# Optimization experiments

Measured on AMD Instinct MI355X. Metric: run time of the kernel, lower is better.

The kernel has to match this reference:

```python
import jax, jax.numpy as jnp
import numpy as np

SCALE = 1.0 / np.sqrt(512.0).astype(np.float32)  # attention() hardcodes d_k=512


def setup_inputs() -> dict:
    key = jax.random.key(0)
    ks = jax.random.split(key, 9)
    B, S, D = 4, 2048, 512
    mk = lambda k, shape: jax.random.normal(k, shape, dtype=jnp.float32) * 0.05
    return {
        "q": mk(ks[0], (B, S, D)),
        "k": mk(ks[1], (B, S, D)),
        "v": mk(ks[2], (B, S, D)),
        "WQ_w": mk(ks[3], (D, D)),
        "WQ_b": mk(ks[4], (D,)),
        "WK_w": mk(ks[5], (D, D)),
        "WK_b": mk(ks[6], (D,)),
        "WV_w": mk(ks[7], (D, D)),
        "WV_b": mk(ks[8], (D,)),
    }


def reference(q, k, v, WQ_w, WQ_b, WK_w, WK_b, WV_w, WV_b):
    # torch nn.Linear: y = x @ W.T + b
    qp = q @ WQ_w.T + WQ_b  # [B,S,dk]
    kp = k @ WK_w.T + WK_b  # [B,S,dk]
    vp = v @ WV_w.T + WV_b  # [B,S,dv]
    qk = jnp.einsum("bqd,bkd->bqk", qp, kp) * SCALE  # [B,Sq,Sk]
    S = qk.shape[1]
    tril = jnp.tril(jnp.ones((S, S), dtype=qk.dtype))  # multiplicative causal mask
    qk = qk * tril
    # NOTE: original applies softmax over dim=1 (the query axis), faithfully kept.
    attn = jax.nn.softmax(qk, axis=1)
    out = jnp.einsum("bqk,bkd->bqd", attn, vp)  # [B,Sq,dv]
    return out
```

## Files before the change

kernel.cpp:

```cpp
#include <hip/hip_runtime.h>
#include <hip/hip_bf16.h>


#define S_LEN 2048
#define D_DIM 512
#define SCALE_F 0.044194173824159216f

typedef __attribute__((ext_vector_type(8))) short s8v;
typedef __attribute__((ext_vector_type(4))) short s4v;
typedef __attribute__((ext_vector_type(4))) float f4v;

enum { EPI_BIAS = 0, EPI_BIAS_T = 1, EPI_SCORES = 2 };

#define SBAR()    asm volatile("s_barrier" ::: "memory")
#define WAITV(n)  asm volatile("s_waitcnt vmcnt(" #n ")" ::: "memory")

__device__ __forceinline__ short f2bf_s(float f) {
  union { __hip_bfloat16 b; short s; } u; u.b = __float2bfloat16(f); return u.s;
}
__device__ __forceinline__ float bf2f_s(short h) {
  union { short s; __hip_bfloat16 b; } u; u.s = h; return __bfloat162float(u.b);
}

__device__ __forceinline__ void glds16(const short* g, short* l) {
  __builtin_amdgcn_global_load_lds((const __attribute__((address_space(1))) void*)g,
                                   (__attribute__((address_space(3))) void*)l, 16, 0, 0);
}

template <int EPI>
__device__ __forceinline__ void gemm_core(
    const short* __restrict__ A, const short* __restrict__ B,
    short* __restrict__ C, const float* __restrict__ bias,
    short* SMEM, int N, int K, size_t sCz, int m0, int n0, int bz,
    float* __restrict__ Z)
{
  const int tid  = threadIdx.x;
  const int w    = tid >> 6;
  const int lane = tid & 63;
  const int quad = lane >> 4;
  const int l16  = lane & 15;
  const int wm   = (w >> 1) * 64;
  const int wn   = (w & 1) * 64;

  const int strow = tid >> 3;
  const int gl = ((tid & 7) ^ (strow & 7)) * 8;

  f4v acc[4][4];
#pragma unroll
  for (int i = 0; i < 4; ++i)
#pragma unroll
    for (int j = 0; j < 4; ++j)
#pragma unroll
      for (int r = 0; r < 4; ++r) acc[i][j][r] = 0.0f;

  const short* Ag = A + (size_t)(m0 + strow) * K + gl;
  const short* Bg = B + (size_t)(n0 + strow) * K + gl;
  const size_t pstr = (size_t)32 * K;
  const int t8 = tid * 8;
  const int swq = l16 & 7;

  const int niter = K >> 6;

#pragma unroll
  for (int p = 0; p < 4; ++p) glds16(Ag + p * pstr, SMEM + t8 + p * 2048);
#pragma unroll
  for (int p = 0; p < 4; ++p) glds16(Bg + p * pstr, SMEM + 8192 + t8 + p * 2048);

  for (int i = 0; i < niter; ++i) {
    const int c = i & 1;
    if (i + 1 < niter) {
      const int k1 = (i + 1) << 6;
      short* dA = SMEM + (1 - c) * 16384 + t8;
#pragma unroll
      for (int p = 0; p < 4; ++p) glds16(Ag + k1 + p * pstr, dA + p * 2048);
#pragma unroll
      for (int p = 0; p < 4; ++p) glds16(Bg + k1 + p * pstr, dA + 8192 + p * 2048);
      WAITV(8);
    } else {
      WAITV(0);
    }
    SBAR();

    const short* As = SMEM + c * 16384;
    const short* Bs = As + 8192;
#pragma unroll
    for (int kk = 0; kk < 2; ++kk) {
      s8v af[4], bf[4];
#pragma unroll
      for (int ii = 0; ii < 4; ++ii)
        af[ii] = *(const s8v*)&As[(wm + ii * 16 + l16) * 64 + (((kk * 4 + quad) ^ swq) * 8)];
#pragma unroll
      for (int j = 0; j < 4; ++j)
        bf[j] = *(const s8v*)&Bs[(wn + j * 16 + l16) * 64 + (((kk * 4 + quad) ^ swq) * 8)];
#pragma unroll
      for (int ii = 0; ii < 4; ++ii)
#pragma unroll
        for (int j = 0; j < 4; ++j)
          acc[ii][j] = __builtin_amdgcn_mfma_f32_16x16x32_bf16(af[ii], bf[j], acc[ii][j], 0, 0, 0);
    }
    SBAR();
  }

  float bv[4];
  if (EPI == EPI_BIAS || EPI == EPI_BIAS_T) {
#pragma unroll
    for (int j = 0; j < 4; ++j) bv[j] = bias[n0 + wn + j * 16 + l16];
  }

  if (EPI == EPI_BIAS_T) {
#pragma unroll
    for (int i = 0; i < 4; ++i) {
#pragma unroll
      for (int j = 0; j < 4; ++j) {
        const int gn  = n0 + wn + j * 16 + l16;
        const int gmb = m0 + wm + i * 16 + quad * 4;
        const int bb = gmb >> 11, ssb = gmb & (S_LEN - 1);
        s4v o;
#pragma unroll
        for (int r = 0; r < 4; ++r) o[r] = f2bf_s(acc[i][j][r] + bv[j]);
        *(s4v*)&C[((size_t)bb * D_DIM + gn) * S_LEN + ssb] = o;
      }
    }
    return;
  }

  short* TB = SMEM;
  const int wbase = w * 2176;
  float csum[4] = {0.f, 0.f, 0.f, 0.f};

#pragma unroll
  for (int ph = 0; ph < 2; ++ph) {
    __syncthreads();
#pragma unroll
    for (int ii = 0; ii < 2; ++ii) {
      const int i = ph * 2 + ii;
#pragma unroll
      for (int j = 0; j < 4; ++j) {
        const int gn = n0 + wn + j * 16 + l16;
#pragma unroll
        for (int r = 0; r < 4; ++r) {
          short o;
          if (EPI == EPI_SCORES) {
            const int gm = m0 + wm + i * 16 + quad * 4 + r;
            const float f = (gm >= gn) ? (__expf(acc[i][j][r] * SCALE_F) - 1.0f) : 0.0f;
            csum[j] += f;
            o = f2bf_s(f);
          } else {
            o = f2bf_s(acc[i][j][r] + bv[j]);
          }
          TB[wbase + (ii * 16 + quad * 4 + r) * 68 + j * 16 + l16] = o;
        }
      }
    }
    __syncthreads();
#pragma unroll
    for (int p = 0; p < 4; ++p) {
      const int row = p * 8 + (lane >> 3);
      const int cg  = lane & 7;
      const s8v vv = *(const s8v*)&TB[wbase + row * 68 + cg * 8];
      const int gm = m0 + wm + ph * 32 + row;
      const int gn = n0 + wn + cg * 8;
      *(s8v*)&C[sCz + (size_t)gm * N + gn] = vv;
    }
  }

  if (EPI == EPI_SCORES) {
#pragma unroll
    for (int j = 0; j < 4; ++j) {
      float cs = csum[j];
      cs += __shfl_xor(cs, 16, 64);
      cs += __shfl_xor(cs, 32, 64);
      if (quad == 0) atomicAdd(&Z[(bz << 11) + n0 + wn + j * 16 + l16], cs);
    }
  }
}

__global__ __launch_bounds__(256, 2) void gemm_scoresF(
    const short* __restrict__ A, const short* __restrict__ B, short* __restrict__ C,
    float* __restrict__ Z)
{
  __shared__ __align__(16) short SMEM[32768];
  const int bz = blockIdx.z;
  const int t = blockIdx.x;
  int ti = (int)((sqrtf(8.0f * t + 1.0f) - 1.0f) * 0.5f);
  while ((ti + 1) * (ti + 2) / 2 <= t) ++ti;
  while (ti * (ti + 1) / 2 > t) --ti;
  const int tj = t - ti * (ti + 1) / 2;
  gemm_core<EPI_SCORES>(A + (size_t)bz * S_LEN * D_DIM, B + (size_t)bz * S_LEN * D_DIM,
                        C, nullptr, SMEM, S_LEN, D_DIM,
                        (size_t)bz * S_LEN * S_LEN, ti * 128, tj * 128, bz, Z);
}

__global__ __launch_bounds__(256, 2) void proj3(
    const short* __restrict__ a0, const short* __restrict__ a1, const short* __restrict__ a2,
    const short* __restrict__ b0, const short* __restrict__ b1, const short* __restrict__ b2,
    short* __restrict__ c0, short* __restrict__ c1, short* __restrict__ c2,
    const float* __restrict__ x0, const float* __restrict__ x1, const float* __restrict__ x2)
{
  __shared__ __align__(16) short SMEM[32768];
  const int z = blockIdx.z;
  const short* A = (z == 0) ? a0 : (z == 1) ? a1 : a2;
  const short* B = (z == 0) ? b0 : (z == 1) ? b1 : b2;
  short*       C = (z == 0) ? c0 : (z == 1) ? c1 : c2;
  const float* bias = (z == 0) ? x0 : (z == 1) ? x1 : x2;
  if (z == 2)
    gemm_core<EPI_BIAS_T>(A, B, C, bias, SMEM, D_DIM, D_DIM, 0,
                          blockIdx.y * 128, blockIdx.x * 128, 0, nullptr);
  else
    gemm_core<EPI_BIAS>(A, B, C, bias, SMEM, D_DIM, D_DIM, 0,
                        blockIdx.y * 128, blockIdx.x * 128, 0, nullptr);
}

__global__ __launch_bounds__(256, 2) void gemm_outF(
    const short* __restrict__ F, const short* __restrict__ vpT,
    const float* __restrict__ Tv, float* __restrict__ out)
{
  __shared__ __align__(16) short SMEM[36864];

  const int tid  = threadIdx.x;
  const int bz   = blockIdx.z;
  const int m0   = (31 - blockIdx.y) * 64;
  const int n0   = blockIdx.x * 128;

  const short* A = F   + (size_t)bz * S_LEN * S_LEN;
  const short* B = vpT + (size_t)bz * D_DIM * S_LEN;

  const int w    = tid >> 6;
  const int lane = tid & 63;
  const int quad = lane >> 4;
  const int l16  = lane & 15;
  const int wm   = (w >> 1) * 32;
  const int wn   = (w & 1) * 64;

  const int strow = tid >> 3;
  const int gl = ((tid & 7) ^ (strow & 7)) * 8;

  f4v acc[2][4];
#pragma unroll
  for (int i = 0; i < 2; ++i)
#pragma unroll
    for (int j = 0; j < 4; ++j)
#pragma unroll
      for (int r = 0; r < 4; ++r) acc[i][j][r] = 0.0f;

  const short* Ag = A + (size_t)(m0 + strow) * S_LEN + gl;
  const short* Bg = B + (size_t)(n0 + strow) * S_LEN + gl;
  const size_t pstr = (size_t)32 * S_LEN;
  const int t8 = tid * 8;
  const int swq = l16 & 7;

  const int niter = (m0 >> 6) + 1;

#pragma unroll
  for (int pre = 0; pre < 2; ++pre) {
    short* dst = SMEM + pre * 12288 + t8;
    const int k0 = pre << 6;
#pragma unroll
    for (int p = 0; p < 2; ++p) glds16(Ag + k0 + p * pstr, dst + p * 2048);
#pragma unroll
    for (int p = 0; p < 4; ++p) glds16(Bg + k0 + p * pstr, dst + 4096 + p * 2048);
  }

  int cbuf = 0, nbuf = 2;
  for (int i = 0; i < niter; ++i) {
    if (i + 2 < niter) {
      const int k2 = (i + 2) << 6;
      short* dst = SMEM + nbuf * 12288 + t8;
#pragma unroll
      for (int p = 0; p < 2; ++p) glds16(Ag + k2 + p * pstr, dst + p * 2048);
#pragma unroll
      for (int p = 0; p < 4; ++p) glds16(Bg + k2 + p * pstr, dst + 4096 + p * 2048);
      nbuf = (nbuf == 2) ? 0 : nbuf + 1;
      WAITV(12);
    } else if (i + 1 < niter) {
      WAITV(6);
    } else {
      WAITV(0);
    }
    SBAR();

    const short* As = SMEM + cbuf * 12288;
    const short* Bs = As + 4096;
    cbuf = (cbuf == 2) ? 0 : cbuf + 1;
#pragma unroll
    for (int kk = 0; kk < 2; ++kk) {
      s8v af[2], bf[4];
#pragma unroll
      for (int ii = 0; ii < 2; ++ii)
        af[ii] = *(const s8v*)&As[(wm + ii * 16 + l16) * 64 + (((kk * 4 + quad) ^ swq) * 8)];
#pragma unroll
      for (int j = 0; j < 4; ++j)
        bf[j] = *(const s8v*)&Bs[(wn + j * 16 + l16) * 64 + (((kk * 4 + quad) ^ swq) * 8)];
#pragma unroll
      for (int ii = 0; ii < 2; ++ii)
#pragma unroll
        for (int j = 0; j < 4; ++j)
          acc[ii][j] = __builtin_amdgcn_mfma_f32_16x16x32_bf16(af[ii], bf[j], acc[ii][j], 0, 0, 0);
    }
    SBAR();
  }

  float* Cf = out + (size_t)bz * S_LEN * D_DIM;
#pragma unroll
  for (int i = 0; i < 2; ++i) {
#pragma unroll
    for (int j = 0; j < 4; ++j) {
      const int gn = n0 + wn + j * 16 + l16;
      const float tvn = Tv[(bz << 9) + gn];
#pragma unroll
      for (int r = 0; r < 4; ++r) {
        const int gm = m0 + wm + i * 16 + quad * 4 + r;
        Cf[(size_t)gm * D_DIM + gn] = acc[i][j][r] + tvn;
      }
    }
  }
}

__global__ __launch_bounds__(256) void cvt3(
    const float* __restrict__ s0, const float* __restrict__ s1,
    const float* __restrict__ s2, short* __restrict__ dst, int n)
{
  const float* s = (blockIdx.y == 0) ? s0 : (blockIdx.y == 1) ? s1 : s2;
  short* d = dst + (size_t)blockIdx.y * n;
  const int i = (blockIdx.x * 256 + threadIdx.x) * 8;
  if (i >= n) return;
  const float4 f0 = *(const float4*)(s + i);
  const float4 f1 = *(const float4*)(s + i + 4);
  s8v o;
  o[0] = f2bf_s(f0.x); o[1] = f2bf_s(f0.y); o[2] = f2bf_s(f0.z); o[3] = f2bf_s(f0.w);
  o[4] = f2bf_s(f1.x); o[5] = f2bf_s(f1.y); o[6] = f2bf_s(f1.z); o[7] = f2bf_s(f1.w);
  *(s8v*)(d + i) = o;
}

__global__ __launch_bounds__(256) void scale_vpt_T(
    short* __restrict__ vpT, const float* __restrict__ ZF, float* __restrict__ Tv)
{
  __shared__ float red[4];
  const int b = blockIdx.y, d = blockIdx.x, tid = threadIdx.x;
  const size_t rowbase = ((size_t)(b * D_DIM + d)) * S_LEN;
  const float* zf = ZF + (b << 11);
  const int k0 = tid * 8;

  s8v v = *(s8v*)&vpT[rowbase + k0];
  float s = 0.0f;
#pragma unroll
  for (int i = 0; i < 8; ++i) {
    const float w = bf2f_s(v[i]) / (2048.0f + zf[k0 + i]);
    s += w;
    v[i] = f2bf_s(w);
  }
  *(s8v*)&vpT[rowbase + k0] = v;

#pragma unroll
  for (int off = 32; off >= 1; off >>= 1) s += __shfl_xor(s, off, 64);
  if ((tid & 63) == 0) red[tid >> 6] = s;
  __syncthreads();
  if (tid == 0) Tv[(b << 9) + d] = red[0] + red[1] + red[2] + red[3];
}

extern "C" void kernel_launch(void* const* d_in, const int* in_sizes, int n_in,
                              void* d_out, int out_size, void* d_ws, size_t ws_size,
                              hipStream_t stream) {
  const float* q   = (const float*)d_in[0];
  const float* k   = (const float*)d_in[1];
  const float* v   = (const float*)d_in[2];
  const float* WQw = (const float*)d_in[3];
  const float* WQb = (const float*)d_in[4];
  const float* WKw = (const float*)d_in[5];
  const float* WKb = (const float*)d_in[6];
  const float* WVw = (const float*)d_in[7];
  const float* WVb = (const float*)d_in[8];

  char* ws = (char*)d_ws;
  short* F   = (short*)(ws);
  short* qb  = (short*)(ws);
  short* Wqb = (short*)(ws + 25165824);
  short* qp  = (short*)(ws + 33554432);
  short* kp  = (short*)(ws + 41943040);
  short* vpT = (short*)(ws + 50331648);
  float* ZF  = (float*)(ws + 58720256);
  float* Tv  = (float*)(ws + 58753024);
  short* kb  = qb + 4194304;
  short* vb  = qb + 8388608;
  short* Wkb = Wqb + 262144;
  short* Wvb = Wqb + 524288;

  const dim3 blk(256);

  hipMemsetAsync(ZF, 0, 4 * S_LEN * sizeof(float), stream);

  cvt3<<<dim3(2048, 3), blk, 0, stream>>>(q, k, v, qb, 4194304);
  cvt3<<<dim3(128, 3), blk, 0, stream>>>(WQw, WKw, WVw, Wqb, 262144);

  proj3<<<dim3(4, 64, 3), blk, 0, stream>>>(
      qb, kb, vb, Wqb, Wkb, Wvb, qp, kp, vpT, WQb, WKb, WVb);

  gemm_scoresF<<<dim3(136, 1, 4), blk, 0, stream>>>(qp, kp, F, ZF);

  scale_vpt_T<<<dim3(512, 4), blk, 0, stream>>>(vpT, ZF, Tv);

  gemm_outF<<<dim3(4, 32, 4), blk, 0, stream>>>(F, vpT, Tv, (float*)d_out);
}
```

Measured before the change: 183.2 us.

## Use 64x128 GEMM tiles, replace atomic column sums with per-tile partials

```diff
diff --git a/kernel.cpp b/kernel.cpp
--- a/kernel.cpp
+++ b/kernel.cpp
@@ -27,27 +27,27 @@
                                    (__attribute__((address_space(3))) void*)l, 16, 0, 0);
 }
 
-template <int EPI>
+template <int EPI, int NI>
 __device__ __forceinline__ void gemm_core(
     const short* __restrict__ A, const short* __restrict__ B,
     short* __restrict__ C, const float* __restrict__ bias,
     short* SMEM, int N, int K, size_t sCz, int m0, int n0, int bz,
-    float* __restrict__ Z)
+    float* __restrict__ ZP)
 {
   const int tid  = threadIdx.x;
   const int w    = tid >> 6;
   const int lane = tid & 63;
   const int quad = lane >> 4;
   const int l16  = lane & 15;
-  const int wm   = (w >> 1) * 64;
+  const int wm   = (w >> 1) * (NI * 16);
   const int wn   = (w & 1) * 64;
 
   const int strow = tid >> 3;
   const int gl = ((tid & 7) ^ (strow & 7)) * 8;
 
-  f4v acc[4][4];
-#pragma unroll
-  for (int i = 0; i < 4; ++i)
+  f4v acc[NI][4];
+#pragma unroll
+  for (int i = 0; i < NI; ++i)
 #pragma unroll
     for (int j = 0; j < 4; ++j)
 #pragma unroll
@@ -58,42 +58,44 @@
   const size_t pstr = (size_t)32 * K;
   const int t8 = tid * 8;
   const int swq = l16 & 7;
+  constexpr int ABUF = NI * 2048;
+  constexpr int BUFS = ABUF + 8192;
 
   const int niter = K >> 6;
 
 #pragma unroll
-  for (int p = 0; p < 4; ++p) glds16(Ag + p * pstr, SMEM + t8 + p * 2048);
-#pragma unroll
-  for (int p = 0; p < 4; ++p) glds16(Bg + p * pstr, SMEM + 8192 + t8 + p * 2048);
+  for (int p = 0; p < NI; ++p) glds16(Ag + p * pstr, SMEM + t8 + p * 2048);
+#pragma unroll
+  for (int p = 0; p < 4; ++p) glds16(Bg + p * pstr, SMEM + ABUF + t8 + p * 2048);
 
   for (int i = 0; i < niter; ++i) {
     const int c = i & 1;
     if (i + 1 < niter) {
       const int k1 = (i + 1) << 6;
-      short* dA = SMEM + (1 - c) * 16384 + t8;
-#pragma unroll
-      for (int p = 0; p < 4; ++p) glds16(Ag + k1 + p * pstr, dA + p * 2048);
-#pragma unroll
-      for (int p = 0; p < 4; ++p) glds16(Bg + k1 + p * pstr, dA + 8192 + p * 2048);
-      WAITV(8);
+      short* dst = SMEM + (1 - c) * BUFS + t8;
+#pragma unroll
+      for (int p = 0; p < NI; ++p) glds16(Ag + k1 + p * pstr, dst + p * 2048);
+#pragma unroll
+      for (int p = 0; p < 4; ++p) glds16(Bg + k1 + p * pstr, dst + ABUF + p * 2048);
+      if constexpr (NI == 4) { WAITV(8); } else { WAITV(6); }
     } else {
       WAITV(0);
     }
     SBAR();
 
-    const short* As = SMEM + c * 16384;
-    const short* Bs = As + 8192;
+    const short* As = SMEM + c * BUFS;
+    const short* Bs = As + ABUF;
 #pragma unroll
     for (int kk = 0; kk < 2; ++kk) {
-      s8v af[4], bf[4];
-#pragma unroll
-      for (int ii = 0; ii < 4; ++ii)
+      s8v af[NI], bf[4];
+#pragma unroll
+      for (int ii = 0; ii < NI; ++ii)
         af[ii] = *(const s8v*)&As[(wm + ii * 16 + l16) * 64 + (((kk * 4 + quad) ^ swq) * 8)];
 #pragma unroll
       for (int j = 0; j < 4; ++j)
         bf[j] = *(const s8v*)&Bs[(wn + j * 16 + l16) * 64 + (((kk * 4 + quad) ^ swq) * 8)];
 #pragma unroll
-      for (int ii = 0; ii < 4; ++ii)
+      for (int ii = 0; ii < NI; ++ii)
 #pragma unroll
         for (int j = 0; j < 4; ++j)
           acc[ii][j] = __builtin_amdgcn_mfma_f32_16x16x32_bf16(af[ii], bf[j], acc[ii][j], 0, 0, 0);
@@ -109,7 +111,7 @@
 
   if (EPI == EPI_BIAS_T) {
 #pragma unroll
-    for (int i = 0; i < 4; ++i) {
+    for (int i = 0; i < NI; ++i) {
 #pragma unroll
       for (int j = 0; j < 4; ++j) {
         const int gn  = n0 + wn + j * 16 + l16;
@@ -129,7 +131,7 @@
   float csum[4] = {0.f, 0.f, 0.f, 0.f};
 
 #pragma unroll
-  for (int ph = 0; ph < 2; ++ph) {
+  for (int ph = 0; ph < NI / 2; ++ph) {
     __syncthreads();
 #pragma unroll
     for (int ii = 0; ii < 2; ++ii) {
@@ -165,50 +167,56 @@
   }
 
   if (EPI == EPI_SCORES) {
+    float* LZ = (float*)(SMEM + 20480);
 #pragma unroll
     for (int j = 0; j < 4; ++j) {
       float cs = csum[j];
       cs += __shfl_xor(cs, 16, 64);
       cs += __shfl_xor(cs, 32, 64);
-      if (quad == 0) atomicAdd(&Z[(bz << 11) + n0 + wn + j * 16 + l16], cs);
-    }
-  }
-}
-
-__global__ __launch_bounds__(256, 2) void gemm_scoresF(
+      if (quad == 0) LZ[(w >> 1) * 128 + wn + j * 16 + l16] = cs;
+    }
+    __syncthreads();
+    if (tid < 128)
+      ZP[(((bz << 5) + (m0 >> 6)) << 11) + n0 + tid] = LZ[tid] + LZ[128 + tid];
+  }
+}
+
+__global__ __launch_bounds__(256, 3) void gemm_scoresF(
     const short* __restrict__ A, const short* __restrict__ B, short* __restrict__ C,
-    float* __restrict__ Z)
-{
-  __shared__ __align__(16) short SMEM[32768];
+    float* __restrict__ ZP)
+{
+  __shared__ __align__(16) short SMEM[24576];
   const int bz = blockIdx.z;
   const int t = blockIdx.x;
-  int ti = (int)((sqrtf(8.0f * t + 1.0f) - 1.0f) * 0.5f);
-  while ((ti + 1) * (ti + 2) / 2 <= t) ++ti;
-  while (ti * (ti + 1) / 2 > t) --ti;
-  const int tj = t - ti * (ti + 1) / 2;
-  gemm_core<EPI_SCORES>(A + (size_t)bz * S_LEN * D_DIM, B + (size_t)bz * S_LEN * D_DIM,
-                        C, nullptr, SMEM, S_LEN, D_DIM,
-                        (size_t)bz * S_LEN * S_LEN, ti * 128, tj * 128, bz, Z);
-}
-
-__global__ __launch_bounds__(256, 2) void proj3(
+  int j = (int)((sqrtf(4.0f * t + 1.0f) - 1.0f) * 0.5f);
+  while ((j + 1) * (j + 2) <= t) ++j;
+  while (j * (j + 1) > t) --j;
+  const int off = t - j * (j + 1);
+  const int ti = (off < j + 1) ? 2 * j : 2 * j + 1;
+  const int tc = (off < j + 1) ? off : off - (j + 1);
+  gemm_core<EPI_SCORES, 2>(A + (size_t)bz * S_LEN * D_DIM, B + (size_t)bz * S_LEN * D_DIM,
+                           C, nullptr, SMEM, S_LEN, D_DIM,
+                           (size_t)bz * S_LEN * S_LEN, ti * 64, tc * 128, bz, ZP);
+}
+
+__global__ __launch_bounds__(256, 3) void proj3(
     const short* __restrict__ a0, const short* __restrict__ a1, const short* __restrict__ a2,
     const short* __restrict__ b0, const short* __restrict__ b1, const short* __restrict__ b2,
     short* __restrict__ c0, short* __restrict__ c1, short* __restrict__ c2,
     const float* __restrict__ x0, const float* __restrict__ x1, const float* __restrict__ x2)
 {
-  __shared__ __align__(16) short SMEM[32768];
+  __shared__ __align__(16) short SMEM[24576];
   const int z = blockIdx.z;
   const short* A = (z == 0) ? a0 : (z == 1) ? a1 : a2;
   const short* B = (z == 0) ? b0 : (z == 1) ? b1 : b2;
   short*       C = (z == 0) ? c0 : (z == 1) ? c1 : c2;
   const float* bias = (z == 0) ? x0 : (z == 1) ? x1 : x2;
   if (z == 2)
-    gemm_core<EPI_BIAS_T>(A, B, C, bias, SMEM, D_DIM, D_DIM, 0,
-                          blockIdx.y * 128, blockIdx.x * 128, 0, nullptr);
+    gemm_core<EPI_BIAS_T, 2>(A, B, C, bias, SMEM, D_DIM, D_DIM, 0,
+                             blockIdx.y * 64, blockIdx.x * 128, 0, nullptr);
   else
-    gemm_core<EPI_BIAS>(A, B, C, bias, SMEM, D_DIM, D_DIM, 0,
-                        blockIdx.y * 128, blockIdx.x * 128, 0, nullptr);
+    gemm_core<EPI_BIAS, 2>(A, B, C, bias, SMEM, D_DIM, D_DIM, 0,
+                           blockIdx.y * 64, blockIdx.x * 128, 0, nullptr);
 }
 
 __global__ __launch_bounds__(256, 2) void gemm_outF(
@@ -316,14 +324,24 @@
   }
 }
 
-__global__ __launch_bounds__(256) void cvt3(
-    const float* __restrict__ s0, const float* __restrict__ s1,
-    const float* __restrict__ s2, short* __restrict__ dst, int n)
-{
-  const float* s = (blockIdx.y == 0) ? s0 : (blockIdx.y == 1) ? s1 : s2;
-  short* d = dst + (size_t)blockIdx.y * n;
-  const int i = (blockIdx.x * 256 + threadIdx.x) * 8;
-  if (i >= n) return;
+__global__ __launch_bounds__(256) void cvt6(
+    const float* __restrict__ q, const float* __restrict__ k, const float* __restrict__ v,
+    const float* __restrict__ wq, const float* __restrict__ wk, const float* __restrict__ wv,
+    short* __restrict__ dstBig, short* __restrict__ dstW)
+{
+  const int y = blockIdx.y;
+  const float* s;
+  short* d;
+  int i;
+  if (blockIdx.x < 2048) {
+    s = (y == 0) ? q : (y == 1) ? k : v;
+    d = dstBig + (size_t)y * 4194304;
+    i = (blockIdx.x * 256 + threadIdx.x) * 8;
+  } else {
+    s = (y == 0) ? wq : (y == 1) ? wk : wv;
+    d = dstW + (size_t)y * 262144;
+    i = ((blockIdx.x - 2048) * 256 + threadIdx.x) * 8;
+  }
   const float4 f0 = *(const float4*)(s + i);
   const float4 f1 = *(const float4*)(s + i + 4);
   s8v o;
@@ -332,23 +350,37 @@
   *(s8v*)(d + i) = o;
 }
 
+__global__ __launch_bounds__(256) void zfin(
+    const float* __restrict__ ZP, float* __restrict__ rsZ)
+{
+  const int idx = blockIdx.x * 256 + threadIdx.x;
+  const int b = idx >> 11, kk = idx & (S_LEN - 1);
+  float s = 2048.0f;
+  for (int i = 2 * (kk >> 7); i < 32; ++i)
+    s += ZP[(((b << 5) + i) << 11) + kk];
+  rsZ[idx] = 1.0f / s;
+}
+
 __global__ __launch_bounds__(256) void scale_vpt_T(
-    short* __restrict__ vpT, const float* __restrict__ ZF, float* __restrict__ Tv)
+    short* __restrict__ vpT, const float* __restrict__ rsZ, float* __restrict__ Tv)
 {
   __shared__ float red[4];
   const int b = blockIdx.y, d = blockIdx.x, tid = threadIdx.x;
   const size_t rowbase = ((size_t)(b * D_DIM + d)) * S_LEN;
-  const float* zf = ZF + (b << 11);
+  const float* rz = rsZ + (b << 11);
   const int k0 = tid * 8;
 
+  const float4 z0 = *(const float4*)&rz[k0];
+  const float4 z1 = *(const float4*)&rz[k0 + 4];
   s8v v = *(s8v*)&vpT[rowbase + k0];
   float s = 0.0f;
-#pragma unroll
-  for (int i = 0; i < 8; ++i) {
-    const float w = bf2f_s(v[i]) / (2048.0f + zf[k0 + i]);
-    s += w;
-    v[i] = f2bf_s(w);
-  }
+  float wv0 = bf2f_s(v[0]) * z0.x, wv1 = bf2f_s(v[1]) * z0.y;
+  float wv2 = bf2f_s(v[2]) * z0.z, wv3 = bf2f_s(v[3]) * z0.w;
+  float wv4 = bf2f_s(v[4]) * z1.x, wv5 = bf2f_s(v[5]) * z1.y;
+  float wv6 = bf2f_s(v[6]) * z1.z, wv7 = bf2f_s(v[7]) * z1.w;
+  s = ((wv0 + wv1) + (wv2 + wv3)) + ((wv4 + wv5) + (wv6 + wv7));
+  v[0] = f2bf_s(wv0); v[1] = f2bf_s(wv1); v[2] = f2bf_s(wv2); v[3] = f2bf_s(wv3);
+  v[4] = f2bf_s(wv4); v[5] = f2bf_s(wv5); v[6] = f2bf_s(wv6); v[7] = f2bf_s(wv7);
   *(s8v*)&vpT[rowbase + k0] = v;
 
 #pragma unroll
@@ -378,8 +410,9 @@
   short* qp  = (short*)(ws + 33554432);
   short* kp  = (short*)(ws + 41943040);
   short* vpT = (short*)(ws + 50331648);
-  float* ZF  = (float*)(ws + 58720256);
-  float* Tv  = (float*)(ws + 58753024);
+  float* ZP  = (float*)(ws + 58720256);
+  float* rsZ = (float*)(ws + 59768832);
+  float* Tv  = (float*)(ws + 59801600);
   short* kb  = qb + 4194304;
   short* vb  = qb + 8388608;
   short* Wkb = Wqb + 262144;
@@ -387,17 +420,16 @@
 
   const dim3 blk(256);
 
-  hipMemsetAsync(ZF, 0, 4 * S_LEN * sizeof(float), stream);
-
-  cvt3<<<dim3(2048, 3), blk, 0, stream>>>(q, k, v, qb, 4194304);
-  cvt3<<<dim3(128, 3), blk, 0, stream>>>(WQw, WKw, WVw, Wqb, 262144);
-
-  proj3<<<dim3(4, 64, 3), blk, 0, stream>>>(
+  cvt6<<<dim3(2176, 3), blk, 0, stream>>>(q, k, v, WQw, WKw, WVw, qb, Wqb);
+
+  proj3<<<dim3(4, 128, 3), blk, 0, stream>>>(
       qb, kb, vb, Wqb, Wkb, Wvb, qp, kp, vpT, WQb, WKb, WVb);
 
-  gemm_scoresF<<<dim3(136, 1, 4), blk, 0, stream>>>(qp, kp, F, ZF);
-
-  scale_vpt_T<<<dim3(512, 4), blk, 0, stream>>>(vpT, ZF, Tv);
+  gemm_scoresF<<<dim3(272, 1, 4), blk, 0, stream>>>(qp, kp, F, ZP);
+
+  zfin<<<dim3(32), blk, 0, stream>>>(ZP, rsZ);
+
+  scale_vpt_T<<<dim3(512, 4), blk, 0, stream>>>(vpT, rsZ, Tv);
 
   gemm_outF<<<dim3(4, 32, 4), blk, 0, stream>>>(F, vpT, Tv, (float*)d_out);
 }
```

Result: slower. 187.6 us (+2.4%).
